# Kernel tuning notes

Measured on AMD Instinct MI355X. Metric: run time of the kernel, lower is better.

## Reference

```python
import jax, jax.numpy as jnp
import numpy as np

H = 1.0  # RBF bandwidth (init kwarg h)


def setup_inputs() -> dict:
    key = jax.random.key(0)
    k1, k2 = jax.random.split(key)
    x = jax.random.normal(k1, (8192, 512), dtype=jnp.float32)
    x1 = jax.random.normal(k2, (8192, 512), dtype=jnp.float32)
    return {"x": x, "x1": x1}


def reference(x, x1):
    # exp(-||x_i - x1_j||^2 / h), computed via the GEMM trick to avoid the
    # O(N*M*D) broadcast intermediate the original torch code materializes.
    x_sq = jnp.sum(x * x, axis=-1, keepdims=True)          # [N, 1]
    x1_sq = jnp.sum(x1 * x1, axis=-1)                       # [M]
    cross = jnp.einsum('nd,md->nm', x, x1)                  # [N, M]
    d = jnp.maximum(x_sq + x1_sq[None, :] - 2.0 * cross, 0.0)
    return jnp.exp(-d / H)
```

## Files before the change

### kernel.cpp

```cpp
#include <hip/hip_runtime.h>
#include <stdint.h>
#include <stddef.h>


#define NROWS 8192
#define DIMK  512
#define BM    128
#define BN    128
#define BKB   128
#define KT    (DIMK / BKB)

typedef __bf16 bf16x8 __attribute__((ext_vector_type(8)));
typedef int    i32x8  __attribute__((ext_vector_type(8)));
typedef int    i32x4  __attribute__((ext_vector_type(4)));
typedef float  f32x4  __attribute__((ext_vector_type(4)));

#define AS1 __attribute__((address_space(1)))
#define AS3 __attribute__((address_space(3)))

__device__ __forceinline__ uint32_t f2bf(float f) {
    uint32_t u = __float_as_uint(f);
    return (u + 0x7FFFu + ((u >> 16) & 1u)) >> 16;
}

__device__ __forceinline__ uint32_t pk_fp8x4(float a, float b, float c, float d) {
    int w = __builtin_amdgcn_cvt_pk_fp8_f32(a, b, 0, false);
    w     = __builtin_amdgcn_cvt_pk_fp8_f32(c, d, w, true);
    return (uint32_t)w;
}

__device__ __forceinline__ i32x8 ld_frag(const uint8_t* base, int c_lo, int c_hi) {
    i32x4 lo = *(const i32x4*)(base + c_lo);
    i32x4 hi = *(const i32x4*)(base + c_hi);
    i32x8 r;
    r[0] = lo[0]; r[1] = lo[1]; r[2] = lo[2]; r[3] = lo[3];
    r[4] = hi[0]; r[5] = hi[1]; r[6] = hi[2]; r[7] = hi[3];
    return r;
}

__global__ __launch_bounds__(256) void precast_fp8(
    const float* __restrict__ x, const float* __restrict__ x1,
    uint8_t* __restrict__ xf, uint8_t* __restrict__ x1f,
    float* __restrict__ xsq, float* __restrict__ x1sq)
{
    const int w    = threadIdx.x >> 6;
    const int lane = threadIdx.x & 63;
    const int row  = blockIdx.x * 4 + w;
    const float* src;
    uint8_t* dstb;
    float* dsts;
    if (blockIdx.y == 0) { src = x  + (size_t)row * DIMK; dstb = xf  + (size_t)row * DIMK; dsts = xsq  + row; }
    else                 { src = x1 + (size_t)row * DIMK; dstb = x1f + (size_t)row * DIMK; dsts = x1sq + row; }

    float4 v0 = ((const float4*)src)[lane * 2];
    float4 v1 = ((const float4*)src)[lane * 2 + 1];
    float s = v0.x * v0.x + v0.y * v0.y + v0.z * v0.z + v0.w * v0.w
            + v1.x * v1.x + v1.y * v1.y + v1.z * v1.z + v1.w * v1.w;

    uint2 p;
    p.x = pk_fp8x4(v0.x, v0.y, v0.z, v0.w);
    p.y = pk_fp8x4(v1.x, v1.y, v1.z, v1.w);
    ((uint2*)dstb)[lane] = p;

    #pragma unroll
    for (int off = 32; off > 0; off >>= 1) s += __shfl_down(s, off);
    if (lane == 0) *dsts = s;
}

__global__ __launch_bounds__(256) void norms_only(
    const float* __restrict__ x, const float* __restrict__ x1,
    float* __restrict__ xsq, float* __restrict__ x1sq)
{
    const int row = blockIdx.x;
    const float* src = (blockIdx.y == 0) ? x + (size_t)row * DIMK : x1 + (size_t)row * DIMK;
    float* dsts      = (blockIdx.y == 0) ? xsq + row : x1sq + row;
    const int t = threadIdx.x;
    float2 v = ((const float2*)src)[t];
    float s = v.x * v.x + v.y * v.y;
    #pragma unroll
    for (int off = 32; off > 0; off >>= 1) s += __shfl_down(s, off);
    __shared__ float red[4];
    if ((t & 63) == 0) red[t >> 6] = s;
    __syncthreads();
    if (t == 0) *dsts = red[0] + red[1] + red[2] + red[3];
}

__global__ __launch_bounds__(256) void rbf_mfma_mxfp8(
    const uint8_t* __restrict__ Xf, const uint8_t* __restrict__ X1f,
    const float* __restrict__ xsq, const float* __restrict__ x1sq,
    float* __restrict__ out)
{
    __shared__ uint8_t As[BM * BKB];
    __shared__ uint8_t Bs[BN * BKB];

    const int t    = threadIdx.x;
    const int bm   = blockIdx.x;
    const int bn   = blockIdx.y;
    const int lane = t & 63;
    const int w    = t >> 6;
    const int wm   = w >> 1;
    const int wn   = w & 1;

    const int srow   = t >> 3;
    const int schunk = (t & 7) ^ (srow & 7);
    const uint8_t* gA = Xf  + (size_t)(bm * BM + srow) * DIMK + schunk * 16;
    const uint8_t* gB = X1f + (size_t)(bn * BN + srow) * DIMK + schunk * 16;
    uint8_t* lA = &As[t * 16];
    uint8_t* lB = &Bs[t * 16];

    const int lrow = lane & 15;
    const int row0 = bm * BM + wm * 64 + (lane >> 4) * 4;
    const int col0 = bn * BN + wn * 64 + lrow;
    float xs[4][4], x1s[4];
    #pragma unroll
    for (int tm = 0; tm < 4; ++tm)
        #pragma unroll
        for (int r = 0; r < 4; ++r) xs[tm][r] = xsq[row0 + tm * 16 + r];
    #pragma unroll
    for (int tn = 0; tn < 4; ++tn) x1s[tn] = x1sq[col0 + tn * 16];

    f32x4 acc[4][4];
    #pragma unroll
    for (int i = 0; i < 4; ++i)
        #pragma unroll
        for (int j = 0; j < 4; ++j)
            acc[i][j] = f32x4{0.f, 0.f, 0.f, 0.f};

    const int q    = lane >> 4;
    const int s    = lrow & 7;
    const int c_lo = ((2 * q)     ^ s) * 16;
    const int c_hi = ((2 * q + 1) ^ s) * 16;
    int roff[4];
    #pragma unroll
    for (int i = 0; i < 4; ++i) roff[i] = (i * 16 + lrow) * BKB;

    #pragma unroll
    for (int kt = 0; kt < KT; ++kt) {
        const uint8_t* ga = gA + kt * BKB;
        const uint8_t* gb = gB + kt * BKB;
        #pragma unroll
        for (int c = 0; c < 4; ++c) {
            __builtin_amdgcn_global_load_lds((AS1 void*)(ga + (size_t)c * 32 * DIMK),
                                             (AS3 void*)(lA + c * 4096), 16, 0, 0);
            __builtin_amdgcn_global_load_lds((AS1 void*)(gb + (size_t)c * 32 * DIMK),
                                             (AS3 void*)(lB + c * 4096), 16, 0, 0);
        }
        __syncthreads();

        i32x8 af[4], bg[4];
        #pragma unroll
        for (int i = 0; i < 4; ++i)
            af[i] = ld_frag(&As[wm * 64 * BKB + roff[i]], c_lo, c_hi);
        #pragma unroll
        for (int i = 0; i < 4; ++i)
            bg[i] = ld_frag(&Bs[wn * 64 * BKB + roff[i]], c_lo, c_hi);
        #pragma unroll
        for (int i = 0; i < 4; ++i)
            #pragma unroll
            for (int j = 0; j < 4; ++j)
                acc[i][j] = __builtin_amdgcn_mfma_scale_f32_16x16x128_f8f6f4(
                    af[i], bg[j], acc[i][j],
                    0, 0,
                    0, 0x7F7F7F7F,
                    0, 0x7F7F7F7F);
        __syncthreads();
    }

    #pragma unroll
    for (int tm = 0; tm < 4; ++tm)
        #pragma unroll
        for (int tn = 0; tn < 4; ++tn)
            #pragma unroll
            for (int r = 0; r < 4; ++r) {
                const int row = row0 + tm * 16 + r;
                const int col = col0 + tn * 16;
                float d = xs[tm][r] + x1s[tn] - 2.0f * acc[tm][tn][r];
                d = fmaxf(d, 0.0f);
                out[(size_t)row * NROWS + col] = __expf(-d);
            }
}

__global__ __launch_bounds__(256) void rbf_mfma_inline(
    const float* __restrict__ X, const float* __restrict__ X1,
    const float* __restrict__ xsq, const float* __restrict__ x1sq,
    float* __restrict__ out)
{
    __shared__ uint16_t As[BM * 32];
    __shared__ uint16_t Bs[BN * 32];

    const int t    = threadIdx.x;
    const int bm   = blockIdx.x;
    const int bn   = blockIdx.y;
    const int lane = t & 63;
    const int w    = t >> 6;
    const int wm   = w >> 1;
    const int wn   = w & 1;

    f32x4 acc[4][4];
    #pragma unroll
    for (int i = 0; i < 4; ++i)
        #pragma unroll
        for (int j = 0; j < 4; ++j)
            acc[i][j] = f32x4{0.f, 0.f, 0.f, 0.f};

    const int lrow = lane & 15;
    const int kq   = (lane >> 4) * 8;
    int aoff[4], boff[4];
    #pragma unroll
    for (int i = 0; i < 4; ++i) {
        aoff[i] = (wm * 64 + i * 16 + lrow) * 32 + kq;
        boff[i] = (wn * 64 + i * 16 + lrow) * 32 + kq;
    }

    #pragma unroll 1
    for (int kt = 0; kt < DIMK / 32; ++kt) {
        #pragma unroll
        for (int i = 0; i < 4; ++i) {
            const int g   = t + i * 256;
            const int row = g >> 3;
            const int c4  = (g & 7) * 4;
            float4 va = *(const float4*)&X [(size_t)(bm * BM + row) * DIMK + kt * 32 + c4];
            float4 vb = *(const float4*)&X1[(size_t)(bn * BN + row) * DIMK + kt * 32 + c4];
            uint2 pa, pb;
            pa.x = f2bf(va.x) | (f2bf(va.y) << 16);
            pa.y = f2bf(va.z) | (f2bf(va.w) << 16);
            pb.x = f2bf(vb.x) | (f2bf(vb.y) << 16);
            pb.y = f2bf(vb.z) | (f2bf(vb.w) << 16);
            *(uint2*)&As[g * 4] = pa;
            *(uint2*)&Bs[g * 4] = pb;
        }
        __syncthreads();

        bf16x8 af[4], bg[4];
        #pragma unroll
        for (int i = 0; i < 4; ++i) af[i] = *(const bf16x8*)&As[aoff[i]];
        #pragma unroll
        for (int i = 0; i < 4; ++i) bg[i] = *(const bf16x8*)&Bs[boff[i]];
        #pragma unroll
        for (int i = 0; i < 4; ++i)
            #pragma unroll
            for (int j = 0; j < 4; ++j)
                acc[i][j] = __builtin_amdgcn_mfma_f32_16x16x32_bf16(af[i], bg[j], acc[i][j], 0, 0, 0);
        __syncthreads();
    }

    const int row0 = bm * BM + wm * 64 + (lane >> 4) * 4;
    const int col0 = bn * BN + wn * 64 + lrow;
    float xs[4][4], x1s[4];
    #pragma unroll
    for (int tm = 0; tm < 4; ++tm)
        #pragma unroll
        for (int r = 0; r < 4; ++r) xs[tm][r] = xsq[row0 + tm * 16 + r];
    #pragma unroll
    for (int tn = 0; tn < 4; ++tn) x1s[tn] = x1sq[col0 + tn * 16];

    #pragma unroll
    for (int tm = 0; tm < 4; ++tm)
        #pragma unroll
        for (int tn = 0; tn < 4; ++tn)
            #pragma unroll
            for (int r = 0; r < 4; ++r) {
                const int row = row0 + tm * 16 + r;
                const int col = col0 + tn * 16;
                float d = xs[tm][r] + x1s[tn] - 2.0f * acc[tm][tn][r];
                d = fmaxf(d, 0.0f);
                out[(size_t)row * NROWS + col] = __expf(-d);
            }
}

extern "C" void kernel_launch(void* const* d_in, const int* in_sizes, int n_in,
                              void* d_out, int out_size, void* d_ws, size_t ws_size,
                              hipStream_t stream)
{
    const float* x  = (const float*)d_in[0];
    const float* x1 = (const float*)d_in[1];
    float* out = (float*)d_out;

    const size_t f8_bytes  = (size_t)NROWS * DIMK;
    const size_t need_full = 2 * f8_bytes + 2 * (size_t)NROWS * sizeof(float);

    dim3 gridG(NROWS / BM, NROWS / BN);

    if (ws_size >= need_full) {
        uint8_t* xf   = (uint8_t*)d_ws;
        uint8_t* x1f  = xf + f8_bytes;
        float*   xsq  = (float*)((char*)d_ws + 2 * f8_bytes);
        float*   x1sq = xsq + NROWS;
        precast_fp8<<<dim3(NROWS / 4, 2), 256, 0, stream>>>(x, x1, xf, x1f, xsq, x1sq);
        rbf_mfma_mxfp8<<<gridG, 256, 0, stream>>>(xf, x1f, xsq, x1sq, out);
    } else {
        float* xsq  = (float*)d_ws;
        float* x1sq = xsq + NROWS;
        norms_only<<<dim3(NROWS, 2), 256, 0, stream>>>(x, x1, xsq, x1sq);
        rbf_mfma_inline<<<gridG, 256, 0, stream>>>(x, x1, xsq, x1sq, out);
    }
}
```

Baseline: 308.2 us.

## Double-buffer fp8 LDS tiles with manual waitcnt pipelining in MFMA kernel

Splits the shared tiles into two buffers and unrolls the K loop so the next tile's global-to-LDS loads are issued before the current MFMAs run, using explicit vmcnt/lgkmcnt waits and raw barriers. The row-norm loads are moved after the main loop to keep them out of the load counter sequence. It doubles LDS usage, which may lower occupancy, and relies on hand-counted waitcnt values being correct.

```diff
diff --git a/kernel.cpp b/kernel.cpp
--- a/kernel.cpp
+++ b/kernel.cpp
@@ -17,6 +17,10 @@
 
 #define AS1 __attribute__((address_space(1)))
 #define AS3 __attribute__((address_space(3)))
+
+#define WAITV(n) asm volatile("s_waitcnt vmcnt(" #n ")" ::: "memory")
+#define WAITL()  asm volatile("s_waitcnt lgkmcnt(0)" ::: "memory")
+#define BAR()    asm volatile("s_barrier" ::: "memory")
 
 __device__ __forceinline__ uint32_t f2bf(float f) {
     uint32_t u = __float_as_uint(f);
@@ -90,8 +94,8 @@
     const float* __restrict__ xsq, const float* __restrict__ x1sq,
     float* __restrict__ out)
 {
-    __shared__ uint8_t As[BM * BKB];
-    __shared__ uint8_t Bs[BN * BKB];
+    __shared__ uint8_t As[2][BM * BKB];
+    __shared__ uint8_t Bs[2][BN * BKB];
 
     const int t    = threadIdx.x;
     const int bm   = blockIdx.x;
@@ -105,19 +109,6 @@
     const int schunk = (t & 7) ^ (srow & 7);
     const uint8_t* gA = Xf  + (size_t)(bm * BM + srow) * DIMK + schunk * 16;
     const uint8_t* gB = X1f + (size_t)(bn * BN + srow) * DIMK + schunk * 16;
-    uint8_t* lA = &As[t * 16];
-    uint8_t* lB = &Bs[t * 16];
-
-    const int lrow = lane & 15;
-    const int row0 = bm * BM + wm * 64 + (lane >> 4) * 4;
-    const int col0 = bn * BN + wn * 64 + lrow;
-    float xs[4][4], x1s[4];
-    #pragma unroll
-    for (int tm = 0; tm < 4; ++tm)
-        #pragma unroll
-        for (int r = 0; r < 4; ++r) xs[tm][r] = xsq[row0 + tm * 16 + r];
-    #pragma unroll
-    for (int tn = 0; tn < 4; ++tn) x1s[tn] = x1sq[col0 + tn * 16];
 
     f32x4 acc[4][4];
     #pragma unroll
@@ -126,6 +117,7 @@
         for (int j = 0; j < 4; ++j)
             acc[i][j] = f32x4{0.f, 0.f, 0.f, 0.f};
 
+    const int lrow = lane & 15;
     const int q    = lane >> 4;
     const int s    = lrow & 7;
     const int c_lo = ((2 * q)     ^ s) * 16;
@@ -134,26 +126,30 @@
     #pragma unroll
     for (int i = 0; i < 4; ++i) roff[i] = (i * 16 + lrow) * BKB;
 
-    #pragma unroll
-    for (int kt = 0; kt < KT; ++kt) {
+    auto stage = [&](int kt, int b) {
         const uint8_t* ga = gA + kt * BKB;
         const uint8_t* gb = gB + kt * BKB;
+        uint8_t* la = &As[b][t * 16];
+        uint8_t* lb = &Bs[b][t * 16];
         #pragma unroll
         for (int c = 0; c < 4; ++c) {
             __builtin_amdgcn_global_load_lds((AS1 void*)(ga + (size_t)c * 32 * DIMK),
-                                             (AS3 void*)(lA + c * 4096), 16, 0, 0);
+                                             (AS3 void*)(la + c * 4096), 16, 0, 0);
             __builtin_amdgcn_global_load_lds((AS1 void*)(gb + (size_t)c * 32 * DIMK),
-                                             (AS3 void*)(lB + c * 4096), 16, 0, 0);
+                                             (AS3 void*)(lb + c * 4096), 16, 0, 0);
         }
-        __syncthreads();
-
-        i32x8 af[4], bg[4];
+    };
+
+    auto read_frags = [&](int b, i32x8* af, i32x8* bg) {
         #pragma unroll
         for (int i = 0; i < 4; ++i)
-            af[i] = ld_frag(&As[wm * 64 * BKB + roff[i]], c_lo, c_hi);
+            af[i] = ld_frag(&As[b][wm * 64 * BKB + roff[i]], c_lo, c_hi);
         #pragma unroll
         for (int i = 0; i < 4; ++i)
-            bg[i] = ld_frag(&Bs[wn * 64 * BKB + roff[i]], c_lo, c_hi);
+            bg[i] = ld_frag(&Bs[b][wn * 64 * BKB + roff[i]], c_lo, c_hi);
+    };
+
+    auto do_mfma = [&](const i32x8* af, const i32x8* bg) {
         #pragma unroll
         for (int i = 0; i < 4; ++i)
             #pragma unroll
@@ -163,8 +159,42 @@
                     0, 0,
                     0, 0x7F7F7F7F,
                     0, 0x7F7F7F7F);
-        __syncthreads();
-    }
+    };
+
+    i32x8 af[4], bg[4];
+
+    stage(0, 0);
+    stage(1, 1);
+
+    WAITV(8); BAR();
+    read_frags(0, af, bg);
+    WAITL(); BAR();
+    stage(2, 0);
+    do_mfma(af, bg);
+
+    WAITV(8); BAR();
+    read_frags(1, af, bg);
+    WAITL(); BAR();
+    stage(3, 1);
+    do_mfma(af, bg);
+
+    WAITV(8); BAR();
+    read_frags(0, af, bg);
+    do_mfma(af, bg);
+
+    WAITV(0); BAR();
+    read_frags(1, af, bg);
+    do_mfma(af, bg);
+
+    const int row0 = bm * BM + wm * 64 + (lane >> 4) * 4;
+    const int col0 = bn * BN + wn * 64 + lrow;
+    float xs[4][4], x1s[4];
+    #pragma unroll
+    for (int tm = 0; tm < 4; ++tm)
+        #pragma unroll
+        for (int r = 0; r < 4; ++r) xs[tm][r] = xsq[row0 + tm * 16 + r];
+    #pragma unroll
+    for (int tn = 0; tn < 4; ++tn) x1s[tn] = x1sq[col0 + tn * 16];
 
     #pragma unroll
     for (int tm = 0; tm < 4; ++tm)
```

Result: no change. 304.3 us (-1.3%).
